# Optimization experiments

Hardware: AMD Instinct MI355X
Metric: run time of the kernel (lower is better)

## Reference

```python
import jax, jax.numpy as jnp
import numpy as np

N_NODES = 100000
N_EDGES = 1600000
H_DIM = 64
N_LAYERS = 3
NUM_GRAPHS = 256


def setup_inputs() -> dict:
    key = jax.random.key(0)
    ks = jax.random.split(key, 6)
    x = jax.random.normal(ks[0], (N_NODES, H_DIM), dtype=jnp.float32)
    edge_index = jax.random.randint(ks[1], (2, N_EDGES), 0, N_NODES, dtype=jnp.int32)
    batch = jnp.sort(jax.random.randint(ks[2], (N_NODES,), 0, NUM_GRAPHS, dtype=jnp.int32))
    s = 1.0 / np.sqrt(H_DIM)
    weight = jax.random.normal(ks[3], (N_LAYERS, H_DIM, H_DIM), dtype=jnp.float32) * s
    W_ih = jax.random.normal(ks[4], (3 * H_DIM, H_DIM), dtype=jnp.float32) * s
    W_hh = jax.random.normal(ks[5], (3 * H_DIM, H_DIM), dtype=jnp.float32) * s
    b_ih = jnp.zeros((3 * H_DIM,), dtype=jnp.float32)
    b_hh = jnp.zeros((3 * H_DIM,), dtype=jnp.float32)
    return {"x": x, "edge_index": edge_index, "batch": batch, "weight": weight,
            "W_ih": W_ih, "W_hh": W_hh, "b_ih": b_ih, "b_hh": b_hh}


def _gru_cell(m, h, W_ih, W_hh, b_ih, b_hh):
    # torch.nn.GRUCell: gates stacked as [reset, update, new]
    gi = m @ W_ih.T + b_ih  # [N, 3d]
    gh = h @ W_hh.T + b_hh  # [N, 3d]
    i_r, i_z, i_n = jnp.split(gi, 3, axis=-1)
    h_r, h_z, h_n = jnp.split(gh, 3, axis=-1)
    r = jax.nn.sigmoid(i_r + h_r)
    z = jax.nn.sigmoid(i_z + h_z)
    n = jnp.tanh(i_n + r * h_n)
    return (1.0 - z) * n + z * h


def reference(x, edge_index, batch, weight, W_ih, W_hh, b_ih, b_hh):
    src, dst = edge_index[0], edge_index[1]
    h = x  # in_channels == out_channels, no zero-padding needed
    for i in range(N_LAYERS):
        m = h @ weight[i]                       # [N, d] linear transform
        agg = jax.ops.segment_sum(m[src], dst, num_segments=N_NODES)  # gather + scatter-add
        h = _gru_cell(agg, h, W_ih, W_hh, b_ih, b_hh)
    # scatter_sum graph pooling over batch ids
    return jax.ops.segment_sum(h, batch, num_segments=NUM_GRAPHS)  # [num_graphs, d]
```

## Files before the change

kernel.cpp:

```cpp
#include <hip/hip_runtime.h>
#include <math.h>

#define NN 100000
#define NE 1600000
#define HD 64
#define NG 256

typedef _Float16 half2v __attribute__((ext_vector_type(2)));

__device__ __forceinline__ unsigned pkh2(float a, float b) {
    return __builtin_bit_cast(unsigned, __builtin_amdgcn_cvt_pkrtz(a, b));
}

__device__ __forceinline__ float dot2(float acc, unsigned a, unsigned b) {
#if __has_builtin(__builtin_amdgcn_fdot2)
    return __builtin_amdgcn_fdot2(__builtin_bit_cast(half2v, a),
                                  __builtin_bit_cast(half2v, b), acc, false);
#else
    asm("v_dot2_f32_f16 %0, %1, %2, %0" : "+v"(acc) : "v"(a), "v"(b));
    return acc;
#endif
}

__device__ __forceinline__ unsigned rlu(unsigned v, int l) {
    return (unsigned)__builtin_amdgcn_readlane((int)v, l);
}

__global__ __launch_bounds__(256) void k_deg(const int* __restrict__ ei, int* __restrict__ deg) {
    int tid = blockIdx.x * 256 + threadIdx.x;
    int stride = gridDim.x * 256;
    for (int e = tid; e < NE; e += stride)
        atomicAdd(&deg[ei[NE + e]], 1);
}

__global__ __launch_bounds__(1024) void k_scan(const int* __restrict__ deg,
                                               int* __restrict__ cursor) {
    __shared__ int buf[1024];
    __shared__ int s_carry;
    if (threadIdx.x == 0) s_carry = 0;
    __syncthreads();
    for (int base = 0; base < NN; base += 4096) {
        int idx = base + threadIdx.x * 4;
        int d0 = 0, d1 = 0, d2 = 0, d3 = 0;
        if (idx + 3 < NN) {
            const int4 v = *(const int4*)(deg + idx);
            d0 = v.x; d1 = v.y; d2 = v.z; d3 = v.w;
        } else {
            if (idx < NN) d0 = deg[idx];
            if (idx + 1 < NN) d1 = deg[idx + 1];
            if (idx + 2 < NN) d2 = deg[idx + 2];
        }
        int tsum = d0 + d1 + d2 + d3;
        buf[threadIdx.x] = tsum;
        __syncthreads();
        for (int off = 1; off < 1024; off <<= 1) {
            int t = (threadIdx.x >= off) ? buf[threadIdx.x - off] : 0;
            __syncthreads();
            buf[threadIdx.x] += t;
            __syncthreads();
        }
        int incl = buf[threadIdx.x];
        int carry = s_carry;
        int e0 = incl - tsum + carry;
        int e1 = e0 + d0, e2 = e1 + d1, e3 = e2 + d2;
        if (idx < NN)     cursor[idx] = e0;
        if (idx + 1 < NN) cursor[idx + 1] = e1;
        if (idx + 2 < NN) cursor[idx + 2] = e2;
        if (idx + 3 < NN) cursor[idx + 3] = e3;
        __syncthreads();
        if (threadIdx.x == 0) s_carry += buf[1023];
        __syncthreads();
    }
}

__global__ __launch_bounds__(256) void k_fill(const int* __restrict__ ei,
                                              int* __restrict__ cursor,
                                              int2* __restrict__ epack) {
    int tid = blockIdx.x * 256 + threadIdx.x;
    int stride = gridDim.x * 256;
    for (int e = tid; e < NE; e += stride) {
        int s = ei[e];
        int d = ei[NE + e];
        int pos = atomicAdd(&cursor[d], 1);
        epack[pos] = make_int2(s, d);
    }
}

__global__ __launch_bounds__(256) void k_lin(const float* __restrict__ h,
                                             const float* __restrict__ W,
                                             float* __restrict__ m) {
    __shared__ float Wl[HD * HD];
    for (int i = threadIdx.x; i < HD * HD; i += 256) Wl[i] = W[i];
    __syncthreads();
    int lane = threadIdx.x & 63, wid = threadIdx.x >> 6;
    int step = gridDim.x * 4;
    for (int n = blockIdx.x * 4 + wid; n < NN; n += step) {
        float hv = h[(size_t)n * HD + lane];
        float acc = 0.f;
        #pragma unroll
        for (int k = 0; k < HD; ++k)
            acc = fmaf(__shfl(hv, k, 64), Wl[k * HD + lane], acc);
        m[(size_t)n * HD + lane] = acc;
    }
}

__global__ __launch_bounds__(256) void k_lin2(const unsigned* __restrict__ hq,
                                              const float* __restrict__ W,
                                              float* __restrict__ m) {
    __shared__ unsigned WL[32 * 65];
    for (int i = threadIdx.x; i < 32 * 64; i += 256) {
        int kk = i >> 6, c = i & 63;
        WL[kk * 65 + c] = pkh2(W[(2 * kk) * HD + c], W[(2 * kk + 1) * HD + c]);
    }
    __syncthreads();
    int lane = threadIdx.x & 63, wid = threadIdx.x >> 6;
    int step = gridDim.x * 4;
    for (int n = blockIdx.x * 4 + wid; n < NN; n += step) {
        unsigned hv = hq[(size_t)n * 32 + (lane & 31)];
        float acc = 0.f;
        #pragma unroll 8
        for (int kk = 0; kk < 32; ++kk)
            acc = dot2(acc, rlu(hv, kk), WL[kk * 65 + lane]);
        m[(size_t)n * HD + lane] = acc;
    }
}

__global__ __launch_bounds__(256) void k_gather(const float* __restrict__ m,
                                                const int2* __restrict__ epack,
                                                float* __restrict__ agg) {
    int gw = (int)((blockIdx.x * 256 + threadIdx.x) >> 6);
    int lane = threadIdx.x & 63;
    int nw = (gridDim.x * 256) >> 6;
    int per = (NE + nw - 1) / nw;
    int s = gw * per;
    int e = s + per; if (e > NE) e = NE;
    if (s >= NE) return;

    float acc = 0.f;
    int cur = epack[s].y;
    int i = s;
    for (; i + 4 <= e; i += 4) {
        int2 p0 = epack[i], p1 = epack[i + 1], p2 = epack[i + 2], p3 = epack[i + 3];
        float v0 = m[(size_t)p0.x * HD + lane];
        float v1 = m[(size_t)p1.x * HD + lane];
        float v2 = m[(size_t)p2.x * HD + lane];
        float v3 = m[(size_t)p3.x * HD + lane];
        if (p0.y != cur) { atomicAdd(&agg[(size_t)cur * HD + lane], acc); acc = 0.f; cur = p0.y; }
        acc += v0;
        if (p1.y != cur) { atomicAdd(&agg[(size_t)cur * HD + lane], acc); acc = 0.f; cur = p1.y; }
        acc += v1;
        if (p2.y != cur) { atomicAdd(&agg[(size_t)cur * HD + lane], acc); acc = 0.f; cur = p2.y; }
        acc += v2;
        if (p3.y != cur) { atomicAdd(&agg[(size_t)cur * HD + lane], acc); acc = 0.f; cur = p3.y; }
        acc += v3;
    }
    for (; i < e; ++i) {
        int2 p = epack[i];
        float v = m[(size_t)p.x * HD + lane];
        if (p.y != cur) { atomicAdd(&agg[(size_t)cur * HD + lane], acc); acc = 0.f; cur = p.y; }
        acc += v;
    }
    atomicAdd(&agg[(size_t)cur * HD + lane], acc);
}

__global__ __launch_bounds__(256) void k_cell(const float* __restrict__ agg,
                                              const float* __restrict__ Wih,
                                              const float* __restrict__ Whh,
                                              const float* __restrict__ bih,
                                              const float* __restrict__ bhh,
                                              const float* __restrict__ h_in,
                                              float* __restrict__ h_out,
                                              unsigned* __restrict__ hpk_out,
                                              int write_pk) {
    __shared__ unsigned WT[32 * 385];
    const float2* A2 = (const float2*)Wih;
    const float2* H2 = (const float2*)Whh;
    for (int i = threadIdx.x; i < 192 * 32; i += 256) {
        int j = i >> 5, kk = i & 31;
        float2 w = A2[i];
        WT[kk * 385 + j] = pkh2(w.x, w.y);
    }
    for (int i = threadIdx.x; i < 192 * 32; i += 256) {
        int j = i >> 5, kk = i & 31;
        float2 w = H2[i];
        WT[kk * 385 + 192 + j] = pkh2(w.x, w.y);
    }
    __syncthreads();

    int lane = threadIdx.x & 63, wid = threadIdx.x >> 6;
    int step = gridDim.x * 4;
    float bi0 = bih[lane], bi1 = bih[64 + lane], bi2 = bih[128 + lane];
    float bh0 = bhh[lane], bh1 = bhh[64 + lane], bh2 = bhh[128 + lane];

    for (int n = blockIdx.x * 4 + wid; n < NN; n += step) {
        float av = agg[(size_t)n * HD + lane];
        float hv = h_in[(size_t)n * HD + lane];
        unsigned apk = pkh2(av, __shfl_xor(av, 1, 64));
        unsigned hpk = pkh2(hv, __shfl_xor(hv, 1, 64));

        float a0 = bi0, a1 = bi1, a2 = bi2;
        float g0 = bh0, g1 = bh1, g2 = bh2;
        #pragma unroll 8
        for (int kk = 0; kk < 32; ++kk) {
            unsigned au = rlu(apk, 2 * kk);
            unsigned hu = rlu(hpk, 2 * kk);
            const unsigned* w = &WT[kk * 385];
            a0 = dot2(a0, au, w[lane]);
            a1 = dot2(a1, au, w[64 + lane]);
            a2 = dot2(a2, au, w[128 + lane]);
            g0 = dot2(g0, hu, w[192 + lane]);
            g1 = dot2(g1, hu, w[256 + lane]);
            g2 = dot2(g2, hu, w[320 + lane]);
        }

        float r = 1.f / (1.f + expf(-(a0 + g0)));
        float z = 1.f / (1.f + expf(-(a1 + g1)));
        float nq = tanhf(a2 + r * g2);
        float hnew = (1.f - z) * nq + z * hv;
        h_out[(size_t)n * HD + lane] = hnew;

        if (write_pk) {
            unsigned o = pkh2(hnew, __shfl_xor(hnew, 1, 64));
            if (!(lane & 1)) hpk_out[(size_t)n * 32 + (lane >> 1)] = o;
        }
    }
}

__global__ __launch_bounds__(256) void k_pool(const float* __restrict__ h,
                                              const int* __restrict__ batch,
                                              float* __restrict__ out) {
    int gw = (int)((blockIdx.x * 256 + threadIdx.x) >> 6);
    int lane = threadIdx.x & 63;
    int nw = (gridDim.x * 256) >> 6;
    int per = (NN + nw - 1) / nw;
    int s = gw * per;
    int e = s + per; if (e > NN) e = NN;
    if (s >= NN) return;
    float acc = 0.f;
    int cur = batch[s];
    for (int n = s; n < e; ++n) {
        int b = batch[n];
        if (b != cur) {
            atomicAdd(&out[cur * HD + lane], acc);
            acc = 0.f; cur = b;
        }
        acc += h[n * HD + lane];
    }
    atomicAdd(&out[cur * HD + lane], acc);
}

extern "C" void kernel_launch(void* const* d_in, const int* in_sizes, int n_in,
                              void* d_out, int out_size, void* d_ws, size_t ws_size,
                              hipStream_t stream) {
    const float* x      = (const float*)d_in[0];
    const int*   ei     = (const int*)d_in[1];
    const int*   batch  = (const int*)d_in[2];
    const float* weight = (const float*)d_in[3];
    const float* Wih    = (const float*)d_in[4];
    const float* Whh    = (const float*)d_in[5];
    const float* bih    = (const float*)d_in[6];
    const float* bhh    = (const float*)d_in[7];
    float* out = (float*)d_out;

    char* ws = (char*)d_ws;
    const size_t szH = (size_t)NN * HD * sizeof(float);
    const size_t szP = (size_t)NN * 32 * sizeof(unsigned);
    float*    H   = (float*)(ws);
    float*    M   = (float*)(ws + szH);
    float*    AG  = (float*)(ws + 2 * szH);
    unsigned* HP  = (unsigned*)(ws + 3 * szH);
    int*   deg    = (int*)(ws + 3 * szH + szP);
    int*   cursor = deg + NN;
    int2*  epack  = (int2*)(cursor + NN);

    hipMemsetAsync(deg, 0, NN * sizeof(int), stream);
    k_deg<<<2048, 256, 0, stream>>>(ei, deg);
    k_scan<<<1, 1024, 0, stream>>>(deg, cursor);
    k_fill<<<2048, 256, 0, stream>>>(ei, cursor, epack);

    k_lin<<<1024, 256, 0, stream>>>(x, weight, M);
    hipMemsetAsync(AG, 0, szH, stream);
    k_gather<<<2048, 256, 0, stream>>>(M, epack, AG);
    k_cell<<<768, 256, 0, stream>>>(AG, Wih, Whh, bih, bhh, x, H, HP, 1);

    k_lin2<<<1024, 256, 0, stream>>>(HP, weight + HD * HD, M);
    hipMemsetAsync(AG, 0, szH, stream);
    k_gather<<<2048, 256, 0, stream>>>(M, epack, AG);
    k_cell<<<768, 256, 0, stream>>>(AG, Wih, Whh, bih, bhh, H, H, HP, 1);

    k_lin2<<<1024, 256, 0, stream>>>(HP, weight + 2 * HD * HD, M);
    hipMemsetAsync(AG, 0, szH, stream);
    k_gather<<<2048, 256, 0, stream>>>(M, epack, AG);
    k_cell<<<768, 256, 0, stream>>>(AG, Wih, Whh, bih, bhh, H, H, HP, 0);

    hipMemsetAsync(out, 0, (size_t)NG * HD * sizeof(float), stream);
    k_pool<<<512, 256, 0, stream>>>(H, batch, out);
}
```

Measured before the change: 1.036 ms.

## Fuse next-layer linear into GRU cell, store messages as fp16, parallelize scan

Fuses the next layer's linear transform into the GRU cell kernel, so the packed-h buffer and the separate k_lin2 pass go away. Messages are stored as fp16, which halves the bytes read by the random-access edge gather. The single-block serial prefix scan is replaced with a three-kernel multi-block scan, and the cell kernel moves to 512-thread blocks. The risks are fp16 precision loss in the messages and higher shared-memory and register pressure in the cell kernel.

```diff
diff --git a/kernel.cpp b/kernel.cpp
--- a/kernel.cpp
+++ b/kernel.cpp
@@ -5,13 +5,19 @@
 #define NE 1600000
 #define HD 64
 #define NG 256
+#define NSB ((NN + 1023) / 1024)
 
 typedef _Float16 half2v __attribute__((ext_vector_type(2)));
 
 __device__ __forceinline__ unsigned pkh2(float a, float b) {
     return __builtin_bit_cast(unsigned, __builtin_amdgcn_cvt_pkrtz(a, b));
 }
-
+__device__ __forceinline__ unsigned short f2h(float a) {
+    union { _Float16 f; unsigned short s; } c; c.f = (_Float16)a; return c.s;
+}
+__device__ __forceinline__ float h2f(unsigned short s) {
+    union { unsigned short s; _Float16 f; } c; c.s = s; return (float)c.f;
+}
 __device__ __forceinline__ float dot2(float acc, unsigned a, unsigned b) {
 #if __has_builtin(__builtin_amdgcn_fdot2)
     return __builtin_amdgcn_fdot2(__builtin_bit_cast(half2v, a),
@@ -21,7 +27,6 @@
     return acc;
 #endif
 }
-
 __device__ __forceinline__ unsigned rlu(unsigned v, int l) {
     return (unsigned)__builtin_amdgcn_readlane((int)v, l);
 }
@@ -33,44 +38,42 @@
         atomicAdd(&deg[ei[NE + e]], 1);
 }
 
-__global__ __launch_bounds__(1024) void k_scan(const int* __restrict__ deg,
-                                               int* __restrict__ cursor) {
+__global__ __launch_bounds__(1024) void k_scan_a(const int* __restrict__ deg,
+                                                 int* __restrict__ cursor,
+                                                 int* __restrict__ bsum) {
     __shared__ int buf[1024];
-    __shared__ int s_carry;
-    if (threadIdx.x == 0) s_carry = 0;
-    __syncthreads();
-    for (int base = 0; base < NN; base += 4096) {
-        int idx = base + threadIdx.x * 4;
-        int d0 = 0, d1 = 0, d2 = 0, d3 = 0;
-        if (idx + 3 < NN) {
-            const int4 v = *(const int4*)(deg + idx);
-            d0 = v.x; d1 = v.y; d2 = v.z; d3 = v.w;
-        } else {
-            if (idx < NN) d0 = deg[idx];
-            if (idx + 1 < NN) d1 = deg[idx + 1];
-            if (idx + 2 < NN) d2 = deg[idx + 2];
-        }
-        int tsum = d0 + d1 + d2 + d3;
-        buf[threadIdx.x] = tsum;
-        __syncthreads();
-        for (int off = 1; off < 1024; off <<= 1) {
-            int t = (threadIdx.x >= off) ? buf[threadIdx.x - off] : 0;
-            __syncthreads();
-            buf[threadIdx.x] += t;
-            __syncthreads();
-        }
-        int incl = buf[threadIdx.x];
-        int carry = s_carry;
-        int e0 = incl - tsum + carry;
-        int e1 = e0 + d0, e2 = e1 + d1, e3 = e2 + d2;
-        if (idx < NN)     cursor[idx] = e0;
-        if (idx + 1 < NN) cursor[idx + 1] = e1;
-        if (idx + 2 < NN) cursor[idx + 2] = e2;
-        if (idx + 3 < NN) cursor[idx + 3] = e3;
-        __syncthreads();
-        if (threadIdx.x == 0) s_carry += buf[1023];
-        __syncthreads();
-    }
+    int t = threadIdx.x;
+    int idx = blockIdx.x * 1024 + t;
+    int v = (idx < NN) ? deg[idx] : 0;
+    buf[t] = v;
+    __syncthreads();
+    for (int off = 1; off < 1024; off <<= 1) {
+        int x = (t >= off) ? buf[t - off] : 0;
+        __syncthreads();
+        buf[t] += x;
+        __syncthreads();
+    }
+    if (idx < NN) cursor[idx] = buf[t] - v;
+    if (t == 1023) bsum[blockIdx.x] = buf[t];
+}
+__global__ __launch_bounds__(128) void k_scan_b(int* __restrict__ bsum) {
+    __shared__ int buf[128];
+    int t = threadIdx.x;
+    int v = (t < NSB) ? bsum[t] : 0;
+    buf[t] = v;
+    __syncthreads();
+    for (int off = 1; off < 128; off <<= 1) {
+        int x = (t >= off) ? buf[t - off] : 0;
+        __syncthreads();
+        buf[t] += x;
+        __syncthreads();
+    }
+    if (t < NSB) bsum[t] = buf[t] - v;
+}
+__global__ __launch_bounds__(1024) void k_scan_c(int* __restrict__ cursor,
+                                                 const int* __restrict__ bsum) {
+    int idx = blockIdx.x * 1024 + threadIdx.x;
+    if (idx < NN) cursor[idx] += bsum[blockIdx.x];
 }
 
 __global__ __launch_bounds__(256) void k_fill(const int* __restrict__ ei,
@@ -88,7 +91,7 @@
 
 __global__ __launch_bounds__(256) void k_lin(const float* __restrict__ h,
                                              const float* __restrict__ W,
-                                             float* __restrict__ m) {
+                                             unsigned short* __restrict__ m16) {
     __shared__ float Wl[HD * HD];
     for (int i = threadIdx.x; i < HD * HD; i += 256) Wl[i] = W[i];
     __syncthreads();
@@ -100,32 +103,11 @@
         #pragma unroll
         for (int k = 0; k < HD; ++k)
             acc = fmaf(__shfl(hv, k, 64), Wl[k * HD + lane], acc);
-        m[(size_t)n * HD + lane] = acc;
-    }
-}
-
-__global__ __launch_bounds__(256) void k_lin2(const unsigned* __restrict__ hq,
-                                              const float* __restrict__ W,
-                                              float* __restrict__ m) {
-    __shared__ unsigned WL[32 * 65];
-    for (int i = threadIdx.x; i < 32 * 64; i += 256) {
-        int kk = i >> 6, c = i & 63;
-        WL[kk * 65 + c] = pkh2(W[(2 * kk) * HD + c], W[(2 * kk + 1) * HD + c]);
-    }
-    __syncthreads();
-    int lane = threadIdx.x & 63, wid = threadIdx.x >> 6;
-    int step = gridDim.x * 4;
-    for (int n = blockIdx.x * 4 + wid; n < NN; n += step) {
-        unsigned hv = hq[(size_t)n * 32 + (lane & 31)];
-        float acc = 0.f;
-        #pragma unroll 8
-        for (int kk = 0; kk < 32; ++kk)
-            acc = dot2(acc, rlu(hv, kk), WL[kk * 65 + lane]);
-        m[(size_t)n * HD + lane] = acc;
-    }
-}
-
-__global__ __launch_bounds__(256) void k_gather(const float* __restrict__ m,
+        m16[(size_t)n * HD + lane] = f2h(acc);
+    }
+}
+
+__global__ __launch_bounds__(256) void k_gather(const unsigned short* __restrict__ m16,
                                                 const int2* __restrict__ epack,
                                                 float* __restrict__ agg) {
     int gw = (int)((blockIdx.x * 256 + threadIdx.x) >> 6);
@@ -141,10 +123,10 @@
     int i = s;
     for (; i + 4 <= e; i += 4) {
         int2 p0 = epack[i], p1 = epack[i + 1], p2 = epack[i + 2], p3 = epack[i + 3];
-        float v0 = m[(size_t)p0.x * HD + lane];
-        float v1 = m[(size_t)p1.x * HD + lane];
-        float v2 = m[(size_t)p2.x * HD + lane];
-        float v3 = m[(size_t)p3.x * HD + lane];
+        float v0 = h2f(m16[(size_t)p0.x * HD + lane]);
+        float v1 = h2f(m16[(size_t)p1.x * HD + lane]);
+        float v2 = h2f(m16[(size_t)p2.x * HD + lane]);
+        float v3 = h2f(m16[(size_t)p3.x * HD + lane]);
         if (p0.y != cur) { atomicAdd(&agg[(size_t)cur * HD + lane], acc); acc = 0.f; cur = p0.y; }
         acc += v0;
         if (p1.y != cur) { atomicAdd(&agg[(size_t)cur * HD + lane], acc); acc = 0.f; cur = p1.y; }
@@ -156,43 +138,51 @@
     }
     for (; i < e; ++i) {
         int2 p = epack[i];
-        float v = m[(size_t)p.x * HD + lane];
+        float v = h2f(m16[(size_t)p.x * HD + lane]);
         if (p.y != cur) { atomicAdd(&agg[(size_t)cur * HD + lane], acc); acc = 0.f; cur = p.y; }
         acc += v;
     }
     atomicAdd(&agg[(size_t)cur * HD + lane], acc);
 }
 
-__global__ __launch_bounds__(256) void k_cell(const float* __restrict__ agg,
+__global__ __launch_bounds__(512) void k_cell(const float* __restrict__ agg,
                                               const float* __restrict__ Wih,
                                               const float* __restrict__ Whh,
                                               const float* __restrict__ bih,
                                               const float* __restrict__ bhh,
                                               const float* __restrict__ h_in,
                                               float* __restrict__ h_out,
-                                              unsigned* __restrict__ hpk_out,
-                                              int write_pk) {
+                                              const float* __restrict__ Wnext,
+                                              unsigned short* __restrict__ m16_next,
+                                              int has_next) {
     __shared__ unsigned WT[32 * 385];
+    __shared__ unsigned WL[32 * 65];
     const float2* A2 = (const float2*)Wih;
     const float2* H2 = (const float2*)Whh;
-    for (int i = threadIdx.x; i < 192 * 32; i += 256) {
+    for (int i = threadIdx.x; i < 192 * 32; i += 512) {
         int j = i >> 5, kk = i & 31;
         float2 w = A2[i];
         WT[kk * 385 + j] = pkh2(w.x, w.y);
     }
-    for (int i = threadIdx.x; i < 192 * 32; i += 256) {
+    for (int i = threadIdx.x; i < 192 * 32; i += 512) {
         int j = i >> 5, kk = i & 31;
         float2 w = H2[i];
         WT[kk * 385 + 192 + j] = pkh2(w.x, w.y);
     }
+    if (has_next)
+        for (int i = threadIdx.x; i < 32 * 64; i += 512) {
+            int kk = i >> 6, c = i & 63;
+            WL[kk * 65 + c] = pkh2(Wnext[(2 * kk) * HD + c], Wnext[(2 * kk + 1) * HD + c]);
+        }
     __syncthreads();
 
     int lane = threadIdx.x & 63, wid = threadIdx.x >> 6;
-    int step = gridDim.x * 4;
+    int gw = blockIdx.x * 8 + wid;
+    const int nwaves = gridDim.x * 8;
     float bi0 = bih[lane], bi1 = bih[64 + lane], bi2 = bih[128 + lane];
     float bh0 = bhh[lane], bh1 = bhh[64 + lane], bh2 = bhh[128 + lane];
 
-    for (int n = blockIdx.x * 4 + wid; n < NN; n += step) {
+    for (int n = gw; n < NN; n += nwaves) {
         float av = agg[(size_t)n * HD + lane];
         float hv = h_in[(size_t)n * HD + lane];
         unsigned apk = pkh2(av, __shfl_xor(av, 1, 64));
@@ -219,9 +209,13 @@
         float hnew = (1.f - z) * nq + z * hv;
         h_out[(size_t)n * HD + lane] = hnew;
 
-        if (write_pk) {
-            unsigned o = pkh2(hnew, __shfl_xor(hnew, 1, 64));
-            if (!(lane & 1)) hpk_out[(size_t)n * 32 + (lane >> 1)] = o;
+        if (has_next) {
+            unsigned npk = pkh2(hnew, __shfl_xor(hnew, 1, 64));
+            float acc = 0.f;
+            #pragma unroll 8
+            for (int kk = 0; kk < 32; ++kk)
+                acc = dot2(acc, rlu(npk, 2 * kk), WL[kk * 65 + lane]);
+            m16_next[(size_t)n * HD + lane] = f2h(acc);
         }
     }
 }
@@ -264,34 +258,35 @@
 
     char* ws = (char*)d_ws;
     const size_t szH = (size_t)NN * HD * sizeof(float);
-    const size_t szP = (size_t)NN * 32 * sizeof(unsigned);
-    float*    H   = (float*)(ws);
-    float*    M   = (float*)(ws + szH);
-    float*    AG  = (float*)(ws + 2 * szH);
-    unsigned* HP  = (unsigned*)(ws + 3 * szH);
-    int*   deg    = (int*)(ws + 3 * szH + szP);
+    const size_t szM = (size_t)NN * HD * sizeof(unsigned short);
+    float*          H    = (float*)(ws);
+    float*          AG   = (float*)(ws + szH);
+    unsigned short* M16  = (unsigned short*)(ws + 2 * szH);
+    int*   deg    = (int*)(ws + 2 * szH + szM);
     int*   cursor = deg + NN;
-    int2*  epack  = (int2*)(cursor + NN);
+    int*   bsum   = cursor + NN;
+    int2*  epack  = (int2*)(bsum + NSB + 2);
 
     hipMemsetAsync(deg, 0, NN * sizeof(int), stream);
     k_deg<<<2048, 256, 0, stream>>>(ei, deg);
-    k_scan<<<1, 1024, 0, stream>>>(deg, cursor);
+    k_scan_a<<<NSB, 1024, 0, stream>>>(deg, cursor, bsum);
+    k_scan_b<<<1, 128, 0, stream>>>(bsum);
+    k_scan_c<<<NSB, 1024, 0, stream>>>(cursor, bsum);
     k_fill<<<2048, 256, 0, stream>>>(ei, cursor, epack);
 
-    k_lin<<<1024, 256, 0, stream>>>(x, weight, M);
+    k_lin<<<1024, 256, 0, stream>>>(x, weight, M16);
     hipMemsetAsync(AG, 0, szH, stream);
-    k_gather<<<2048, 256, 0, stream>>>(M, epack, AG);
-    k_cell<<<768, 256, 0, stream>>>(AG, Wih, Whh, bih, bhh, x, H, HP, 1);
-
-    k_lin2<<<1024, 256, 0, stream>>>(HP, weight + HD * HD, M);
+    k_gather<<<2048, 256, 0, stream>>>(M16, epack, AG);
+    k_cell<<<512, 512, 0, stream>>>(AG, Wih, Whh, bih, bhh, x, H,
+                                    weight + HD * HD, M16, 1);
     hipMemsetAsync(AG, 0, szH, stream);
-    k_gather<<<2048, 256, 0, stream>>>(M, epack, AG);
-    k_cell<<<768, 256, 0, stream>>>(AG, Wih, Whh, bih, bhh, H, H, HP, 1);
-
-    k_lin2<<<1024, 256, 0, stream>>>(HP, weight + 2 * HD * HD, M);
+    k_gather<<<2048, 256, 0, stream>>>(M16, epack, AG);
+    k_cell<<<512, 512, 0, stream>>>(AG, Wih, Whh, bih, bhh, H, H,
+                                    weight + 2 * HD * HD, M16, 1);
     hipMemsetAsync(AG, 0, szH, stream);
-    k_gather<<<2048, 256, 0, stream>>>(M, epack, AG);
-    k_cell<<<768, 256, 0, stream>>>(AG, Wih, Whh, bih, bhh, H, H, HP, 0);
+    k_gather<<<2048, 256, 0, stream>>>(M16, epack, AG);
+    k_cell<<<512, 512, 0, stream>>>(AG, Wih, Whh, bih, bhh, H, H,
+                                    nullptr, nullptr, 0);
 
     hipMemsetAsync(out, 0, (size_t)NG * HD * sizeof(float), stream);
     k_pool<<<512, 256, 0, stream>>>(H, batch, out);
```

Result: faster. 924.7 us (-10.8%).
